# Performance work log

Hardware: AMD Instinct MI355X
Metric: run time of the kernel (lower is better)

## Reference

```python
import jax, jax.numpy as jnp
import numpy as np
from jax import lax
from jax.scipy.special import logsumexp

C, H, W = 21, 512, 512
ITERS = 5
THETA_GAMMA = 3.0
THETA_ALPHA = 160.0
MAX_RADIUS = 8  # truncation cap for the Gaussian surrogate of the permutohedral filter
# deterministic stand-in for random.sample(range(200,400),1) per iteration
SP_IDS = [250 + 7 * i for i in range(ITERS)]


def _gauss_kernel(sigma):
    radius = min(int(2.0 * sigma + 0.5), MAX_RADIUS)
    t = np.arange(-radius, radius + 1, dtype=np.float32)
    k = np.exp(-0.5 * (t / np.float32(sigma)) ** 2)
    k /= k.sum()
    return jnp.asarray(k)


def _blur(x, k):
    # x: (c,h,w); separable Gaussian blur as surrogate for custom high_dim_filter
    x4 = x[:, None]                      # (c,1,h,w), c acts as batch
    kh = k.reshape(1, 1, -1, 1)
    kw = k.reshape(1, 1, 1, -1)
    y = lax.conv_general_dilated(x4, kh, (1, 1), 'SAME')
    y = lax.conv_general_dilated(y, kw, (1, 1), 'SAME')
    return y[:, 0]


def _sp_containment_update(q, low_w, high_w, sp_map, sp_idx):
    # q: softmax output (c,h,w); sp_map: (h,w) int ids; single clique sp_idx
    cond = (sp_map == sp_idx)                       # (h,w)
    condf = cond.astype(q.dtype)[None]              # (1,h,w) broadcast over c
    q_clique = condf * q                            # masked q
    bool_max = (q == q.max(axis=0, keepdims=True))  # global per-pixel argmax mask
    maxlab = q_clique.max(axis=0, keepdims=True)    # per-pixel max label prob in clique
    l_eq = (bool_max & cond[None]).astype(q.dtype) * q
    A_np = q_clique + maxlab - l_eq                 # "A no padding"
    q_sum = A_np                                    # sum over the single clique
    # per-class logsumexp over the whole plane (zeros outside clique, as in source)
    B_sp = logsumexp(q_clique, axis=(1, 2))         # (c,)
    prod_sp = condf * B_sp[:, None, None]
    B_cont = logsumexp(A_np, axis=(1, 2))           # (c,)
    prod_io = condf * B_cont[:, None, None]         # cond applied twice in source == once
    q_mod = q + (q == 0).astype(q.dtype)
    q_sum = q_sum + (q_sum == 0).astype(q.dtype)
    ft = prod_sp / q_mod
    sp_update = low_w[0][:, None, None] * ft + high_w[0] * (1.0 - ft)
    ft2 = prod_io / q_sum
    cont_update = low_w[1][:, None, None] * ft2 + high_w[1] * (1.0 - ft2)
    return sp_update + cont_update


def setup_inputs() -> dict:
    key = jax.random.key(0)
    k1, k2, k3 = jax.random.split(key, 3)
    unaries = jax.random.normal(k1, (1, H, W, C), dtype=jnp.float32)
    rgb = jax.random.uniform(k2, (1, H, W, 3), dtype=jnp.float32)
    sp_map = jax.random.randint(k3, (1, W, H), 0, 400, dtype=jnp.int32)
    spatial_ker_weights = jnp.eye(C, dtype=jnp.float32)
    bilateral_ker_weights = jnp.eye(C, dtype=jnp.float32)
    complex_rel_low_weights = jnp.ones((2, C), dtype=jnp.float32)
    complex_rel_high_weights = jnp.ones((2,), dtype=jnp.float32)
    compatibility_matrix = -jnp.eye(C, dtype=jnp.float32)
    return {
        'unaries': unaries, 'rgb': rgb, 'sp_map': sp_map,
        'spatial_ker_weights': spatial_ker_weights,
        'bilateral_ker_weights': bilateral_ker_weights,
        'complex_rel_low_weights': complex_rel_low_weights,
        'complex_rel_high_weights': complex_rel_high_weights,
        'compatibility_matrix': compatibility_matrix,
    }


def reference(unaries, rgb, sp_map, spatial_ker_weights, bilateral_ker_weights,
              complex_rel_low_weights, complex_rel_high_weights, compatibility_matrix):
    u = jnp.transpose(unaries[0], (2, 0, 1))   # (c,h,w)
    sp = jnp.transpose(sp_map[0])              # (h,w)
    k_sp = _gauss_kernel(THETA_GAMMA)
    k_bi = _gauss_kernel(THETA_ALPHA)
    ones = jnp.ones((C, H, W), jnp.float32)
    spatial_norm = _blur(ones, k_sp)
    bilateral_norm = _blur(ones, k_bi)
    q = u
    for i in range(ITERS):
        sm = jax.nn.softmax(q, axis=0)
        spatial_out = _blur(sm, k_sp) / spatial_norm
        bilateral_out = _blur(sm, k_bi) / bilateral_norm
        cont = _sp_containment_update(sm, complex_rel_low_weights,
                                      complex_rel_high_weights, sp, SP_IDS[i])
        mp = (jnp.einsum('ij,jhw->ihw', spatial_ker_weights, spatial_out)
              + jnp.einsum('ij,jhw->ihw', bilateral_ker_weights, bilateral_out))
        pairwise = jnp.einsum('ij,jhw->ihw', compatibility_matrix, mp)
        q = u - pairwise - cont
    return jnp.transpose(q, (1, 2, 0))[None]   # (1,h,w,c)
```

## Files before the change

### kernel.cpp

```cpp
#include <hip/hip_runtime.h>
#include <hip/hip_bf16.h>
#include <math.h>
#include <utility>

#define C 21
#define H 512
#define W 512
#define HW (H*W)
#define CHW (C*HW)
#define N_ITERS 5
#define RSP 6
#define KSP 13
#define RBI 8
#define KBI 17
#define LIST_CAP 4096

#define KSP_OFF   0
#define KBI_OFF   16
#define NSP_OFF   64
#define NBI_OFF   576
#define M1_OFF    1088
#define M2_OFF    1536
#define NCOND_OFF 2048
#define S1_OFF    2064
#define S2_OFF    2176
#define LIST_OFF  2304
#define CONTB_OFF 22784
#define UBH_OFF   131072
#define QB16_OFF  (UBH_OFF + CHW/2)
#define T12_OFF   (QB16_OFF + CHW/2)
#define QBF_OFF   (T12_OFF + CHW)

#define REP21(F) F(0) F(1) F(2) F(3) F(4) F(5) F(6) F(7) F(8) F(9) F(10) \
                 F(11) F(12) F(13) F(14) F(15) F(16) F(17) F(18) F(19) F(20)

template <int... Js, typename F>
__device__ __forceinline__ void sfor(std::integer_sequence<int, Js...>, F&& f) {
  (f(std::integral_constant<int, Js>{}), ...);
}
#define SFOR(N, ...) sfor(std::make_integer_sequence<int, N>{}, __VA_ARGS__)

__device__ __forceinline__ float bf2f(unsigned short u) {
  return __uint_as_float(((unsigned)u) << 16);
}
__device__ __forceinline__ unsigned short f2bfu(float a) {
  __hip_bfloat16 h = __float2bfloat16(a);
  return *(unsigned short*)&h;
}
__device__ __forceinline__ unsigned packbf(float a, float b) {
  return (unsigned)f2bfu(a) | ((unsigned)f2bfu(b) << 16);
}

__global__ __launch_bounds__(512) void k_setup(float* ws, const float* skw,
                                               const float* bkw, const float* cm) {
  int tid = threadIdx.x;
  if (tid == 0) {
    float s = 0.f;
    for (int i = 0; i < KSP; ++i) {
      float t = (float)(i - RSP);
      float v = expf(-0.5f * (t / 3.0f) * (t / 3.0f));
      ws[KSP_OFF + i] = v; s += v;
    }
    for (int i = 0; i < KSP; ++i) ws[KSP_OFF + i] /= s;
    s = 0.f;
    for (int i = 0; i < KBI; ++i) {
      float t = (float)(i - RBI);
      float v = expf(-0.5f * (t / 160.0f) * (t / 160.0f));
      ws[KBI_OFF + i] = v; s += v;
    }
    for (int i = 0; i < KBI; ++i) ws[KBI_OFF + i] /= s;
  }
  __syncthreads();
  if (tid < H) {
    float nsp = 0.f, nbi = 0.f;
    for (int t = 0; t < KSP; ++t) { int x = tid + t - RSP; if (x >= 0 && x < H) nsp += ws[KSP_OFF + t]; }
    for (int t = 0; t < KBI; ++t) { int x = tid + t - RBI; if (x >= 0 && x < H) nbi += ws[KBI_OFF + t]; }
    ws[NSP_OFF + tid] = 1.f / nsp;
    ws[NBI_OFF + tid] = 1.f / nbi;
  }
  if (tid < C * C) {
    int i = tid / C, j = tid % C;
    float m1 = 0.f, m2 = 0.f;
    for (int k = 0; k < C; ++k) {
      m1 += cm[i * C + k] * skw[k * C + j];
      m2 += cm[i * C + k] * bkw[k * C + j];
    }
    ws[M1_OFF + tid] = m1;
    ws[M2_OFF + tid] = m2;
  }
  if (tid < N_ITERS * C) { ws[S1_OFF + tid] = 0.f; ws[S2_OFF + tid] = 0.f; }
  if (tid < N_ITERS) ((int*)(ws + NCOND_OFF))[tid] = 0;
}

__global__ __launch_bounds__(256) void k_spt(const int* __restrict__ sp_map,
                                             int* __restrict__ ncond,
                                             int* __restrict__ list) {
  int p = blockIdx.x * 256 + threadIdx.x;
  int h = p >> 9, w = p & 511;
  int v = sp_map[w * H + h];
#pragma unroll
  for (int i = 0; i < N_ITERS; ++i)
    if (v == 250 + 7 * i) {
      int slot = atomicAdd(&ncond[i], 1);
      if (slot < LIST_CAP) list[i * LIST_CAP + slot] = p;
    }
}

__global__ __launch_bounds__(256) void k_tin(const float* __restrict__ in,
                                             unsigned* __restrict__ ubh32,
                                             unsigned* __restrict__ qb32) {
  __shared__ float t[C * 257];
  int tid = threadIdx.x;
  size_t p0 = (size_t)blockIdx.x * 256;
  size_t fbase = p0 * C;
#pragma unroll
  for (int i = 0; i < C; ++i) {
    int e = i * 256 + tid;
    int p = e / C, c = e % C;
    t[c * 257 + p] = in[fbase + e];
  }
  __syncthreads();
  if (tid < 128) {
#pragma unroll
    for (int c = 0; c < C; ++c) {
      float v0 = t[c * 257 + 2 * tid];
      float v1 = t[c * 257 + 2 * tid + 1];
      unsigned d = packbf(v0, v1);
      size_t di = ((size_t)c * HW + p0) / 2 + tid;
      ubh32[di] = d;
      qb32[di] = d;
    }
  }
}

__global__ __launch_bounds__(256) void k_tout(const float* __restrict__ qb,
                                              float* __restrict__ out) {
  __shared__ float t[C * 257];
  int tid = threadIdx.x;
  size_t p0 = (size_t)blockIdx.x * 256;
#pragma unroll
  for (int c = 0; c < C; ++c)
    t[c * 257 + tid] = qb[(size_t)c * HW + p0 + tid];
  __syncthreads();
  size_t fbase = p0 * C;
#pragma unroll
  for (int i = 0; i < C; ++i) {
    int e = i * 256 + tid;
    int p = e / C, c = e % C;
    out[fbase + e] = t[c * 257 + p];
  }
}

__global__ __launch_bounds__(256) void k_cliqueA(const unsigned short* __restrict__ qh,
                                                 float* __restrict__ ws, int iter) {
  int tid = threadIdx.x;
  const int* ncond = (const int*)(ws + NCOND_OFF);
  const int* list = (const int*)(ws + LIST_OFF) + iter * LIST_CAP;
  int n = ncond[iter]; if (n > LIST_CAP) n = LIST_CAP;
#define D1(i) float s1_##i = 0.f, s2_##i = 0.f;
  REP21(D1)
#undef D1
  for (int j = blockIdx.x * 256 + tid; j < n; j += 1024) {
    int p = list[j];
#define LQ(i) float q##i = __expf(bf2f(qh[(size_t)(i) * HW + p]));
    REP21(LQ)
#undef LQ
    float s = ((((q0+q1)+(q2+q3))+((q4+q5)+(q6+q7)))+(((q8+q9)+(q10+q11))+((q12+q13)+(q14+q15))))+(((q16+q17)+(q18+q19))+q20);
    float inv = 1.f / s;
    float smax = 0.f;
#define NM(i) q##i *= inv; smax = fmaxf(smax, q##i);
    REP21(NM)
#undef NM
#define AC(i) { s1_##i += __expf(q##i); \
                float A = (q##i == smax) ? smax : q##i + smax; \
                s2_##i += __expf(A); }
    REP21(AC)
#undef AC
  }
#define RED(x) x += __shfl_xor(x, 32); x += __shfl_xor(x, 16); x += __shfl_xor(x, 8); \
               x += __shfl_xor(x, 4); x += __shfl_xor(x, 2); x += __shfl_xor(x, 1);
#define RD(i) RED(s1_##i) RED(s2_##i)
  REP21(RD)
#undef RD
#undef RED
  if ((tid & 63) == 0) {
#define AT(i) atomicAdd(&ws[S1_OFF + iter * C + (i)], s1_##i); \
              atomicAdd(&ws[S2_OFF + iter * C + (i)], s2_##i);
    REP21(AT)
#undef AT
  }
}

__global__ __launch_bounds__(256) void k_cliqueB(const unsigned short* __restrict__ qh,
                                                 float* __restrict__ ws,
                                                 const float* __restrict__ loww,
                                                 const float* __restrict__ highw,
                                                 int iter) {
  int tid = threadIdx.x;
  const int* ncond = (const int*)(ws + NCOND_OFF);
  const int* list = (const int*)(ws + LIST_OFF) + iter * LIST_CAP;
  int n = ncond[iter]; if (n > LIST_CAP) n = LIST_CAP;
  float HWn = (float)(HW - n);
#define LB(i) float lb1_##i = logf(HWn + ws[S1_OFF + iter * C + (i)]); \
              float lb2_##i = logf(HWn + ws[S2_OFF + iter * C + (i)]);
  REP21(LB)
#undef LB
  float high0 = highw[0], high1 = highw[1];
  float* contb = ws + CONTB_OFF;
  for (int j = blockIdx.x * 256 + tid; j < n; j += 1024) {
    int p = list[j];
#define LQ2(i) float q##i = __expf(bf2f(qh[(size_t)(i) * HW + p]));
    REP21(LQ2)
#undef LQ2
    float s = ((((q0+q1)+(q2+q3))+((q4+q5)+(q6+q7)))+(((q8+q9)+(q10+q11))+((q12+q13)+(q14+q15))))+(((q16+q17)+(q18+q19))+q20);
    float inv = 1.f / s;
    float smax = 0.f;
#define NM2(i) q##i *= inv; smax = fmaxf(smax, q##i);
    REP21(NM2)
#undef NM2
#define CW(i) { float A = (q##i == smax) ? smax : q##i + smax; \
                float ft = lb1_##i / q##i; \
                float ft2 = lb2_##i / A; \
                contb[j * C + (i)] = loww[i] * ft + high0 * (1.f - ft) \
                                   + loww[C + (i)] * ft2 + high1 * (1.f - ft2); }
    REP21(CW)
#undef CW
  }
}

__global__ __launch_bounds__(256) void k_smmix(const unsigned* __restrict__ q16x2,
                                               unsigned* __restrict__ t12,
                                               const float* __restrict__ ws) {
  int tid = threadIdx.x;
  int b2 = blockIdx.x * 256 + tid;
#define LQ(i) unsigned d##i = q16x2[(size_t)(i) * (HW/2) + b2]; \
              float ex##i = __expf(__uint_as_float(d##i << 16)); \
              float ey##i = __expf(__uint_as_float(d##i & 0xFFFF0000u));
  REP21(LQ)
#undef LQ
  float sa = ((((ex0+ex1)+(ex2+ex3))+((ex4+ex5)+(ex6+ex7)))+(((ex8+ex9)+(ex10+ex11))+((ex12+ex13)+(ex14+ex15))))+(((ex16+ex17)+(ex18+ex19))+ex20);
  float sb = ((((ey0+ey1)+(ey2+ey3))+((ey4+ey5)+(ey6+ey7)))+(((ey8+ey9)+(ey10+ey11))+((ey12+ey13)+(ey14+ey15))))+(((ey16+ey17)+(ey18+ey19))+ey20);
  float ia = 1.f / sa, ib = 1.f / sb;
#define NQ(i) ex##i *= ia; ey##i *= ib;
  REP21(NQ)
#undef NQ
  for (int i = 0; i < C; ++i) {
    const float* r1 = ws + M1_OFF + i * C;
    const float* r2 = ws + M2_OFF + i * C;
    float t1a = 0.f, t1b = 0.f, t2a = 0.f, t2b = 0.f;
#define MIX(c) { float m1v = r1[c], m2v = r2[c]; \
                 t1a += m1v * ex##c; t1b += m1v * ey##c; \
                 t2a += m2v * ex##c; t2b += m2v * ey##c; }
    REP21(MIX)
#undef MIX
    uint2 st;
    st.x = packbf(t1a, t2a);
    st.y = packbf(t1b, t2b);
    *reinterpret_cast<uint2*>(t12 + (size_t)i * HW + 2 * b2) = st;
  }
}

template <bool LAST>
__global__ __launch_bounds__(256) void k_blur2d(
    const unsigned* __restrict__ t12, const unsigned* __restrict__ uh32,
    void* __restrict__ qout, const float* __restrict__ ws,
    const float* __restrict__ highw) {
  __shared__ float asmem[16 * 152], bsmem[16 * 152];
  __shared__ float ktsp[KSP], ktbi[KBI];
  __shared__ float nspw[128], nbiw[128], nsph[16], nbih[16];
  int tid = threadIdx.x;
  int l = blockIdx.x;
  int nl = (l & 7) * 336 + (l >> 3);
  int c = nl >> 7;
  int rem = nl & 127;
  int h0 = (rem >> 2) * 16;
  int w0 = (rem & 3) * 128;
  if (tid < KSP) ktsp[tid] = ws[KSP_OFF + tid];
  if (tid >= 32 && tid < 32 + KBI) ktbi[tid - 32] = ws[KBI_OFF + tid - 32];
  if (tid >= 64 && tid < 192) {
    int i = tid - 64;
    nspw[i] = ws[NSP_OFF + w0 + i];
    nbiw[i] = ws[NBI_OFF + w0 + i];
  }
  if (tid >= 192 && tid < 208) {
    int i = tid - 192;
    nsph[i] = ws[NSP_OFF + h0 + i];
    nbih[i] = ws[NBI_OFF + h0 + i];
  }
  __syncthreads();
  size_t cbase = (size_t)c * HW;
  if (tid < 144) {
    int col = w0 - 8 + tid;
    bool okc = (col >= 0 && col < W);
    const unsigned* s12 = t12 + cbase;
    unsigned lv[32];
    SFOR(32, [&](auto jc) {
      constexpr int j = decltype(jc)::value;
      int hh = h0 - 8 + j;
      lv[j] = (okc && hh >= 0 && hh < H) ? s12[(size_t)hh * W + col] : 0u;
    });
    float a[16], b[16];
    SFOR(16, [&](auto oc) {
      constexpr int o = decltype(oc)::value;
      a[o] = 0.f; b[o] = 0.f;
    });
    SFOR(32, [&](auto jc) {
      constexpr int j = decltype(jc)::value;
      float f1 = __uint_as_float(lv[j] << 16);
      float f2 = __uint_as_float(lv[j] & 0xFFFF0000u);
      SFOR(16, [&](auto oc) {
        constexpr int o = decltype(oc)::value;
        if constexpr (j - 2 - o >= 0 && j - 2 - o < KSP) a[o] += ktsp[j - 2 - o] * f1;
        if constexpr (j - o >= 0 && j - o < KBI) b[o] += ktbi[j - o] * f2;
      });
    });
    SFOR(16, [&](auto oc) {
      constexpr int o = decltype(oc)::value;
      asmem[o * 152 + tid] = a[o];
      bsmem[o * 152 + tid] = b[o];
    });
  }
  __syncthreads();
  float cc = highw[0] + highw[1];
#pragma unroll
  for (int k = 0; k < 2; ++k) {
    int o = tid + k * 256;
    int r = o >> 5;
    int wq = (o & 31) * 4;
    float aw[16], bw[20];
    const float2* ap = reinterpret_cast<const float2*>(&asmem[r * 152 + wq + 2]);
    const float2* bp = reinterpret_cast<const float2*>(&bsmem[r * 152 + wq]);
    SFOR(8, [&](auto jc) {
      constexpr int j = decltype(jc)::value;
      float2 v = ap[j];
      aw[2 * j] = v.x;
      aw[2 * j + 1] = v.y;
    });
    SFOR(10, [&](auto jc) {
      constexpr int j = decltype(jc)::value;
      float2 v = bp[j];
      bw[2 * j] = v.x;
      bw[2 * j + 1] = v.y;
    });
    float ao[4], bo[4];
    SFOR(4, [&](auto jc) {
      constexpr int j = decltype(jc)::value;
      float s1 = 0.f;
      float s2 = 0.f;
      SFOR(KSP, [&](auto tc) {
        constexpr int t = decltype(tc)::value;
        s1 += ktsp[t] * aw[j + t];
      });
      SFOR(KBI, [&](auto tc) {
        constexpr int t = decltype(tc)::value;
        s2 += ktbi[t] * bw[j + t];
      });
      ao[j] = s1;
      bo[j] = s2;
    });
    size_t idx = cbase + (size_t)(h0 + r) * W + (w0 + wq);
    uint2 uv = *reinterpret_cast<const uint2*>(uh32 + (idx >> 1));
    float u0 = __uint_as_float(uv.x << 16);
    float u1 = __uint_as_float(uv.x & 0xFFFF0000u);
    float u2 = __uint_as_float(uv.y << 16);
    float u3 = __uint_as_float(uv.y & 0xFFFF0000u);
    float nh1 = nsph[r], nh2 = nbih[r];
    float r0 = u0 - (ao[0] * (nh1 * nspw[wq])     + bo[0] * (nh2 * nbiw[wq]))     - cc;
    float r1 = u1 - (ao[1] * (nh1 * nspw[wq + 1]) + bo[1] * (nh2 * nbiw[wq + 1])) - cc;
    float r2 = u2 - (ao[2] * (nh1 * nspw[wq + 2]) + bo[2] * (nh2 * nbiw[wq + 2])) - cc;
    float r3 = u3 - (ao[3] * (nh1 * nspw[wq + 3]) + bo[3] * (nh2 * nbiw[wq + 3])) - cc;
    if constexpr (LAST) {
      *reinterpret_cast<float4*>((float*)qout + idx) = make_float4(r0, r1, r2, r3);
    } else {
      uint2 st;
      st.x = packbf(r0, r1);
      st.y = packbf(r2, r3);
      *reinterpret_cast<uint2*>((unsigned*)qout + (idx >> 1)) = st;
    }
  }
}

template <bool F32Q>
__global__ __launch_bounds__(256) void k_contfix(void* __restrict__ qout,
                                                 const float* __restrict__ ws,
                                                 const float* __restrict__ highw,
                                                 int iter) {
  const int* ncond = (const int*)(ws + NCOND_OFF);
  int n = ncond[iter]; if (n > LIST_CAP) n = LIST_CAP;
  int e = blockIdx.x * 256 + threadIdx.x;
  if (e >= n * C) return;
  int j = e / C, c = e - j * C;
  const int* list = (const int*)(ws + LIST_OFF) + iter * LIST_CAP;
  int p = list[j];
  float cc = highw[0] + highw[1];
  float delta = cc - ws[CONTB_OFF + e];
  size_t idx = (size_t)c * HW + p;
  if constexpr (F32Q) {
    ((float*)qout)[idx] += delta;
  } else {
    unsigned short* q16 = (unsigned short*)qout;
    q16[idx] = f2bfu(bf2f(q16[idx]) + delta);
  }
}

extern "C" void kernel_launch(void* const* d_in, const int* in_sizes, int n_in,
                              void* d_out, int out_size, void* d_ws, size_t ws_size,
                              hipStream_t stream) {
  const float* unaries = (const float*)d_in[0];
  const int* sp_map = (const int*)d_in[2];
  const float* skw = (const float*)d_in[3];
  const float* bkw = (const float*)d_in[4];
  const float* loww = (const float*)d_in[5];
  const float* highw = (const float*)d_in[6];
  const float* cm = (const float*)d_in[7];
  float* out = (float*)d_out;
  float* ws = (float*)d_ws;
  unsigned* ubh32 = (unsigned*)(ws + UBH_OFF);
  unsigned* qb32 = (unsigned*)(ws + QB16_OFF);
  const unsigned short* qh16 = (const unsigned short*)(ws + QB16_OFF);
  unsigned* t12 = (unsigned*)(ws + T12_OFF);
  float* qbf = ws + QBF_OFF;
  int* ncond = (int*)(ws + NCOND_OFF);
  int* list = (int*)(ws + LIST_OFF);

  k_setup<<<1, 512, 0, stream>>>(ws, skw, bkw, cm);
  k_spt<<<HW / 256, 256, 0, stream>>>(sp_map, ncond, list);
  k_tin<<<HW / 256, 256, 0, stream>>>(unaries, ubh32, qb32);
  for (int i = 0; i < N_ITERS; ++i) {
    k_cliqueA<<<4, 256, 0, stream>>>(qh16, ws, i);
    k_cliqueB<<<4, 256, 0, stream>>>(qh16, ws, loww, highw, i);
    k_smmix<<<HW / 512, 256, 0, stream>>>(qb32, t12, ws);
    if (i < N_ITERS - 1) {
      k_blur2d<false><<<2688, 256, 0, stream>>>(t12, ubh32, (void*)qb32, ws, highw);
      k_contfix<false><<<128, 256, 0, stream>>>((void*)qb32, ws, highw, i);
    } else {
      k_blur2d<true><<<2688, 256, 0, stream>>>(t12, ubh32, (void*)qbf, ws, highw);
      k_contfix<true><<<128, 256, 0, stream>>>((void*)qbf, ws, highw, i);
    }
  }
  k_tout<<<HW / 256, 256, 0, stream>>>(qbf, out);
}
```

Before: 379.5 us.

## Fuse setup kernels, merge clique passes via grid barrier, write output directly

Measured after the change: 413.9 us. +9.1%, slower.

```diff
diff --git a/kernel.cpp b/kernel.cpp
--- a/kernel.cpp
+++ b/kernel.cpp
@@ -24,12 +24,12 @@
 #define NCOND_OFF 2048
 #define S1_OFF    2064
 #define S2_OFF    2176
+#define CTR_OFF   2288
 #define LIST_OFF  2304
 #define CONTB_OFF 22784
 #define UBH_OFF   131072
 #define QB16_OFF  (UBH_OFF + CHW/2)
 #define T12_OFF   (QB16_OFF + CHW/2)
-#define QBF_OFF   (T12_OFF + CHW)
 
 #define REP21(F) F(0) F(1) F(2) F(3) F(4) F(5) F(6) F(7) F(8) F(9) F(10) \
                  F(11) F(12) F(13) F(14) F(15) F(16) F(17) F(18) F(19) F(20)
@@ -89,35 +89,38 @@
     ws[M2_OFF + tid] = m2;
   }
   if (tid < N_ITERS * C) { ws[S1_OFF + tid] = 0.f; ws[S2_OFF + tid] = 0.f; }
-  if (tid < N_ITERS) ((int*)(ws + NCOND_OFF))[tid] = 0;
-}
-
-__global__ __launch_bounds__(256) void k_spt(const int* __restrict__ sp_map,
-                                             int* __restrict__ ncond,
-                                             int* __restrict__ list) {
-  int p = blockIdx.x * 256 + threadIdx.x;
-  int h = p >> 9, w = p & 511;
-  int v = sp_map[w * H + h];
-#pragma unroll
-  for (int i = 0; i < N_ITERS; ++i)
-    if (v == 250 + 7 * i) {
-      int slot = atomicAdd(&ncond[i], 1);
-      if (slot < LIST_CAP) list[i * LIST_CAP + slot] = p;
-    }
-}
-
-__global__ __launch_bounds__(256) void k_tin(const float* __restrict__ in,
-                                             unsigned* __restrict__ ubh32,
-                                             unsigned* __restrict__ qb32) {
+  if (tid < N_ITERS) {
+    ((int*)(ws + NCOND_OFF))[tid] = 0;
+    ((int*)(ws + CTR_OFF))[tid] = 0;
+  }
+}
+
+__global__ __launch_bounds__(256) void k_spt_tin(const int* __restrict__ sp_map,
+                                                 const float* __restrict__ in,
+                                                 int* __restrict__ ncond,
+                                                 int* __restrict__ list,
+                                                 unsigned* __restrict__ ubh32,
+                                                 unsigned* __restrict__ qb32) {
   __shared__ float t[C * 257];
   int tid = threadIdx.x;
+  int p = blockIdx.x * 256 + tid;
+  {
+    int h = p >> 9, w = p & 511;
+    int v = sp_map[w * H + h];
+#pragma unroll
+    for (int i = 0; i < N_ITERS; ++i)
+      if (v == 250 + 7 * i) {
+        int slot = atomicAdd(&ncond[i], 1);
+        if (slot < LIST_CAP) list[i * LIST_CAP + slot] = p;
+      }
+  }
   size_t p0 = (size_t)blockIdx.x * 256;
   size_t fbase = p0 * C;
 #pragma unroll
   for (int i = 0; i < C; ++i) {
     int e = i * 256 + tid;
-    int p = e / C, c = e % C;
-    t[c * 257 + p] = in[fbase + e];
+    int pp = e / C, c = e % C;
+    t[c * 257 + pp] = in[fbase + e];
   }
   __syncthreads();
   if (tid < 128) {
@@ -133,26 +136,11 @@
   }
 }
 
-__global__ __launch_bounds__(256) void k_tout(const float* __restrict__ qb,
-                                              float* __restrict__ out) {
-  __shared__ float t[C * 257];
-  int tid = threadIdx.x;
-  size_t p0 = (size_t)blockIdx.x * 256;
-#pragma unroll
-  for (int c = 0; c < C; ++c)
-    t[c * 257 + tid] = qb[(size_t)c * HW + p0 + tid];
-  __syncthreads();
-  size_t fbase = p0 * C;
-#pragma unroll
-  for (int i = 0; i < C; ++i) {
-    int e = i * 256 + tid;
-    int p = e / C, c = e % C;
-    out[fbase + e] = t[c * 257 + p];
-  }
-}
-
-__global__ __launch_bounds__(256) void k_cliqueA(const unsigned short* __restrict__ qh,
-                                                 float* __restrict__ ws, int iter) {
+__global__ __launch_bounds__(256) void k_clique(const unsigned short* __restrict__ qh,
+                                                float* __restrict__ ws,
+                                                const float* __restrict__ loww,
+                                                const float* __restrict__ highw,
+                                                int iter) {
   int tid = threadIdx.x;
   const int* ncond = (const int*)(ws + NCOND_OFF);
   const int* list = (const int*)(ws + LIST_OFF) + iter * LIST_CAP;
@@ -189,17 +177,15 @@
     REP21(AT)
 #undef AT
   }
-}
-
-__global__ __launch_bounds__(256) void k_cliqueB(const unsigned short* __restrict__ qh,
-                                                 float* __restrict__ ws,
-                                                 const float* __restrict__ loww,
-                                                 const float* __restrict__ highw,
-                                                 int iter) {
-  int tid = threadIdx.x;
-  const int* ncond = (const int*)(ws + NCOND_OFF);
-  const int* list = (const int*)(ws + LIST_OFF) + iter * LIST_CAP;
-  int n = ncond[iter]; if (n > LIST_CAP) n = LIST_CAP;
+  __threadfence();
+  __syncthreads();
+  if (tid == 0) {
+    int* ctr = (int*)(ws + CTR_OFF) + iter;
+    atomicAdd(ctr, 1);
+    while (atomicAdd(ctr, 0) < 4) { __builtin_amdgcn_s_sleep(1); }
+  }
+  __syncthreads();
+  __threadfence();
   float HWn = (float)(HW - n);
 #define LB(i) float lb1_##i = logf(HWn + ws[S1_OFF + iter * C + (i)]); \
               float lb2_##i = logf(HWn + ws[S2_OFF + iter * C + (i)]);
@@ -358,7 +344,8 @@
       ao[j] = s1;
       bo[j] = s2;
     });
-    size_t idx = cbase + (size_t)(h0 + r) * W + (w0 + wq);
+    int hh = h0 + r, ww = w0 + wq;
+    size_t idx = cbase + (size_t)hh * W + ww;
     uint2 uv = *reinterpret_cast<const uint2*>(uh32 + (idx >> 1));
     float u0 = __uint_as_float(uv.x << 16);
     float u1 = __uint_as_float(uv.x & 0xFFFF0000u);
@@ -370,7 +357,11 @@
     float r2 = u2 - (ao[2] * (nh1 * nspw[wq + 2]) + bo[2] * (nh2 * nbiw[wq + 2])) - cc;
     float r3 = u3 - (ao[3] * (nh1 * nspw[wq + 3]) + bo[3] * (nh2 * nbiw[wq + 3])) - cc;
     if constexpr (LAST) {
-      *reinterpret_cast<float4*>((float*)qout + idx) = make_float4(r0, r1, r2, r3);
+      float* outp = (float*)qout + ((size_t)hh * W + ww) * C + c;
+      outp[0] = r0;
+      outp[C] = r1;
+      outp[2 * C] = r2;
+      outp[3 * C] = r3;
     } else {
       uint2 st;
       st.x = packbf(r0, r1);
@@ -380,7 +371,7 @@
   }
 }
 
-template <bool F32Q>
+template <bool F32OUT>
 __global__ __launch_bounds__(256) void k_contfix(void* __restrict__ qout,
                                                  const float* __restrict__ ws,
                                                  const float* __restrict__ highw,
@@ -394,11 +385,11 @@
   int p = list[j];
   float cc = highw[0] + highw[1];
   float delta = cc - ws[CONTB_OFF + e];
-  size_t idx = (size_t)c * HW + p;
-  if constexpr (F32Q) {
-    ((float*)qout)[idx] += delta;
+  if constexpr (F32OUT) {
+    ((float*)qout)[(size_t)p * C + c] += delta;
   } else {
     unsigned short* q16 = (unsigned short*)qout;
+    size_t idx = (size_t)c * HW + p;
     q16[idx] = f2bfu(bf2f(q16[idx]) + delta);
   }
 }
@@ -419,24 +410,20 @@
   unsigned* qb32 = (unsigned*)(ws + QB16_OFF);
   const unsigned short* qh16 = (const unsigned short*)(ws + QB16_OFF);
   unsigned* t12 = (unsigned*)(ws + T12_OFF);
-  float* qbf = ws + QBF_OFF;
   int* ncond = (int*)(ws + NCOND_OFF);
   int* list = (int*)(ws + LIST_OFF);
 
   k_setup<<<1, 512, 0, stream>>>(ws, skw, bkw, cm);
-  k_spt<<<HW / 256, 256, 0, stream>>>(sp_map, ncond, list);
-  k_tin<<<HW / 256, 256, 0, stream>>>(unaries, ubh32, qb32);
+  k_spt_tin<<<HW / 256, 256, 0, stream>>>(sp_map, unaries, ncond, list, ubh32, qb32);
   for (int i = 0; i < N_ITERS; ++i) {
-    k_cliqueA<<<4, 256, 0, stream>>>(qh16, ws, i);
-    k_cliqueB<<<4, 256, 0, stream>>>(qh16, ws, loww, highw, i);
+    k_clique<<<4, 256, 0, stream>>>(qh16, ws, loww, highw, i);
     k_smmix<<<HW / 512, 256, 0, stream>>>(qb32, t12, ws);
     if (i < N_ITERS - 1) {
       k_blur2d<false><<<2688, 256, 0, stream>>>(t12, ubh32, (void*)qb32, ws, highw);
       k_contfix<false><<<128, 256, 0, stream>>>((void*)qb32, ws, highw, i);
     } else {
-      k_blur2d<true><<<2688, 256, 0, stream>>>(t12, ubh32, (void*)qbf, ws, highw);
-      k_contfix<true><<<128, 256, 0, stream>>>((void*)qbf, ws, highw, i);
-    }
-  }
-  k_tout<<<HW / 256, 256, 0, stream>>>(qbf, out);
-}
+      k_blur2d<true><<<2688, 256, 0, stream>>>(t12, ubh32, (void*)out, ws, highw);
+      k_contfix<true><<<128, 256, 0, stream>>>((void*)out, ws, highw, i);
+    }
+  }
+}
```
